# Performance work log

Measured on AMD Instinct MI355X. Metric: run time of the kernel, lower is better.

Reference implementation:

```python
import jax, jax.numpy as jnp
import numpy as np

B, C, H, W = 8, 64, 128, 128
K = 3            # deformable kernel size
DIL = 1          # dilation == padding for the deformable conv
OFF_K = 2 * (DIL + 1) + 1   # = 5, offset-conv kernel
OFF_PAD = DIL + 1            # = 2, same-padding for offset conv
KK = K * K


def setup_inputs() -> dict:
    key = jax.random.key(0)
    k1, k2, k3, k4 = jax.random.split(key, 4)
    x = jax.random.normal(k1, (B, C, H, W), dtype=jnp.float32)
    weights = jax.random.normal(k2, (C, C, K, K), dtype=jnp.float32) * 0.05
    offset_w = jax.random.normal(k3, (2 * KK, C, OFF_K, OFF_K), dtype=jnp.float32) * 0.02
    offset_b = jax.random.normal(k4, (2 * KK,), dtype=jnp.float32) * 0.01
    return {"x": x, "weights": weights, "offset_w": offset_w, "offset_b": offset_b}


def _deform_conv2d(x, weights, off):
    # x: [B,C,H,W]; weights: [O,C,K,K]; off: [B,2*KK,H,W] (dy,dx interleaved per tap)
    b, c, h, w = x.shape
    o = weights.shape[0]
    off = off.reshape(b, KK, 2, h, w)
    dy = off[:, :, 0]            # [B,KK,H,W]
    dx = off[:, :, 1]
    ti = jnp.arange(KK) // K     # kernel row per tap
    tj = jnp.arange(KK) % K      # kernel col per tap
    ygrid = jnp.arange(h, dtype=jnp.float32)
    xgrid = jnp.arange(w, dtype=jnp.float32)
    # sample position: out_pos - pad + tap*dilation + offset
    base_y = (ti * DIL - DIL).astype(jnp.float32)  # pad = DIL
    base_x = (tj * DIL - DIL).astype(jnp.float32)
    py = ygrid[None, None, :, None] + base_y[None, :, None, None] + dy  # [B,KK,H,W]
    px = xgrid[None, None, None, :] + base_x[None, :, None, None] + dx

    def sample_one(img, py_b, px_b):
        # img: [C,H,W]; py_b/px_b: [KK,H,W] -> [C,KK,H,W]
        y0 = jnp.floor(py_b)
        x0 = jnp.floor(px_b)
        fy = py_b - y0
        fx = px_b - x0
        y0i = y0.astype(jnp.int32)
        x0i = x0.astype(jnp.int32)

        def corner(yi, xi, wgt):
            valid = (yi >= 0) & (yi < h) & (xi >= 0) & (xi < w)
            v = img[:, jnp.clip(yi, 0, h - 1), jnp.clip(xi, 0, w - 1)]  # [C,KK,H,W]
            return v * (wgt * valid)[None]

        return (corner(y0i, x0i, (1 - fy) * (1 - fx))
                + corner(y0i, x0i + 1, (1 - fy) * fx)
                + corner(y0i + 1, x0i, fy * (1 - fx))
                + corner(y0i + 1, x0i + 1, fy * fx))

    sampled = jax.vmap(sample_one)(x, py, px)            # [B,C,KK,H,W]
    return jnp.einsum('bctyx,oct->boyx', sampled, weights.reshape(o, c, KK))


def reference(x, weights, offset_w, offset_b):
    # offset conv (same padding) + Hardtanh clamp to [-1,1]
    off = jax.lax.conv_general_dilated(
        x, offset_w, window_strides=(1, 1),
        padding=[(OFF_PAD, OFF_PAD), (OFF_PAD, OFF_PAD)],
        dimension_numbers=('NCHW', 'OIHW', 'NCHW'))
    off = off + offset_b[None, :, None, None]
    off = jnp.clip(off, -1.0, 1.0)
    return _deform_conv2d(x, weights, off)
```

## Files before the change

### kernel.cpp

```cpp
#include <hip/hip_runtime.h>

#define BB  8
#define CC  64
#define HH  128
#define WW  128
#define OCC 18
#define XP  133
#define SP  72
#define XTP 68

typedef __attribute__((ext_vector_type(8)))  short bf16x8;
typedef __attribute__((ext_vector_type(16))) float f32x16;

static __device__ __forceinline__ ushort f2bf(float f) {
    union { float f; unsigned u; } v; v.f = f;
    unsigned r = (v.u + 0x7FFFu + ((v.u >> 16) & 1u)) >> 16;
    return (ushort)r;
}
static __device__ __forceinline__ float bfu(unsigned u) {
    union { unsigned u; float f; } v; v.u = u; return v.f;
}

__global__ __launch_bounds__(256) void prep_kernel(
    const float* __restrict__ x, const float* __restrict__ w,
    const float* __restrict__ ow, ushort* __restrict__ XT,
    ushort* __restrict__ WAf, ushort* __restrict__ WDf)
{
    __shared__ ushort T[64 * XTP];
    const int tid = threadIdx.x;
    const int phys = blockIdx.x;

    if (phys >= 2 * BB * HH) {
        int id = phys - 2 * BB * HH;
        if (id < 200) {
            int idx = id * 256 + tid;
            int j  = idx & 7;
            int l  = (idx >> 3) & 63;
            int cs = (idx >> 9) & 3;
            int t  = idx >> 11;
            int oc = l & 31;
            int c  = cs * 16 + (l >> 5) * 8 + j;
            float v = (oc < OCC) ? ow[((size_t)(oc * CC + c)) * 25 + t] : 0.f;
            WAf[idx] = f2bf(v);
        } else {
            int idx = (id - 200) * 256 + tid;
            int j  = idx & 7;
            int l  = (idx >> 3) & 63;
            int cs = (idx >> 9) & 3;
            int mt = (idx >> 11) & 1;
            int t  = idx >> 12;
            int o  = mt * 32 + (l & 31);
            int c  = cs * 16 + (l >> 5) * 8 + j;
            WDf[idx] = f2bf(w[((size_t)(o * CC + c)) * 9 + t]);
        }
        return;
    }

    const int b    = phys & 7;
    const int idx  = phys >> 3;
    const int half = idx & 1;
    const int y    = idx >> 1;

    {
        int j = idx * 256 + tid;
        if (j < 5 * XP * 8) {
            int r   = j / (XP * 8);
            int off = j % (XP * 8);
            int yp  = (r < 2) ? r : (128 + r);
            ((uint4*)(XT + ((size_t)b * XP + yp) * XP * 64))[off] = make_uint4(0, 0, 0, 0);
        }
    }

    const int p   = tid & 63;
    const int ch4 = tid >> 6;
    const float* xb = x + (size_t)b * CC * HH * WW + (size_t)y * WW + half * 64;
#pragma unroll
    for (int i = 0; i < 16; i++) {
        int c = i * 4 + ch4;
        T[p * XTP + c] = f2bf(xb[(size_t)c * HH * WW + p]);
    }
    __syncthreads();

    ushort* orow = XT + (((size_t)b * XP + (y + 2)) * XP) * 64;

    if (half == 0) {
        if (tid < 16) {
            int col = tid >> 3;
            ((uint4*)(orow + (size_t)col * 64))[tid & 7] = make_uint4(0, 0, 0, 0);
        }
    } else {
        if (tid < 24) {
            int col = 130 + (tid >> 3);
            ((uint4*)(orow + (size_t)col * 64))[tid & 7] = make_uint4(0, 0, 0, 0);
        }
    }

#pragma unroll
    for (int g = 0; g < 2; g++) {
        int i2 = g * 256 + tid;
        int pl = i2 >> 3;
        int part = i2 & 7;
        uint2 lo = *(const uint2*)&T[pl * XTP + part * 8];
        uint2 hi = *(const uint2*)&T[pl * XTP + part * 8 + 4];
        uint4 wv; wv.x = lo.x; wv.y = lo.y; wv.z = hi.x; wv.w = hi.y;
        ((uint4*)(orow + ((size_t)(half * 64 + pl + 2)) * 64))[part] = wv;
    }
}

__global__ __launch_bounds__(256, 6) void fused_kernel(
    const ushort* __restrict__ XT, const ushort* __restrict__ WAf,
    const ushort* __restrict__ WDf, const float* __restrict__ ob,
    float* __restrict__ out)
{
    __shared__ __align__(16) char smem[68 * SP * 2];
    __shared__ float off_lds[OCC * 64];

    const int tid   = threadIdx.x;
    const int lane  = tid & 63;
    const int n     = lane & 31;
    const int h     = lane >> 5;
    const int w     = tid >> 6;
    const int ptile = w & 1;
    const int tset  = w >> 1;

    const int b    = blockIdx.x & 7;
    const int idx  = blockIdx.x >> 3;
    const int half = idx & 1;
    const int y    = idx >> 1;

    {
        ushort* XROW = (ushort*)smem;
        float*  red  = (float*)smem;
        f32x16 acc = {};
        const ushort* src0 = XT + (((size_t)b * XP + y) * XP + half * 64) * 64;

        for (int ky = 0; ky < 5; ky++) {
            if (ky) __syncthreads();
            const ushort* src = src0 + (size_t)ky * XP * 64;
            for (int i = tid; i < 68 * 8; i += 256) {
                int pl = i >> 3, ch = (i & 7) * 8;
                *(uint4*)&XROW[pl * SP + ch] = *(const uint4*)(src + (size_t)pl * 64 + ch);
            }
            __syncthreads();

#pragma unroll
            for (int kx = 0; kx < 5; kx++) {
                const int t = ky * 5 + kx;
                const ushort* bbase = &XROW[(ptile * 32 + n + kx) * SP + h * 8];
#pragma unroll
                for (int c2 = 0; c2 < 2; c2++) {
                    const int cs = tset * 2 + c2;
                    bf16x8 af = *(const bf16x8*)(WAf + (((size_t)t * 4 + cs) * 64 + lane) * 8);
                    bf16x8 bf = *(const bf16x8*)(bbase + cs * 16);
                    acc = __builtin_amdgcn_mfma_f32_32x32x16_bf16(af, bf, acc, 0, 0, 0);
                }
            }
        }
        __syncthreads();
        if (tset == 1) {
#pragma unroll
            for (int r = 0; r < 16; r++)
                red[ptile * 1024 + r * 64 + lane] = acc[r];
        }
        __syncthreads();
        if (tset == 0) {
#pragma unroll
            for (int r = 0; r < 16; r++) {
                int oc = (r & 3) + 8 * (r >> 2) + 4 * h;
                if (oc < OCC) {
                    float v = acc[r] + red[ptile * 1024 + r * 64 + lane] + ob[oc];
                    v = fminf(fmaxf(v, -1.f), 1.f);
                    off_lds[oc * 64 + ptile * 32 + n] = v;
                }
            }
        }
        __syncthreads();
    }

    ushort* S = (ushort*)smem;
    const int p   = tid >> 2;
    const int cs4 = (tid & 3) * 16;

    const int m0 = ptile * 32;
    const int n0 = tset * 32;

    f32x16 acc = {};
    const ushort* xtb = XT + (size_t)b * XP * XP * 64;

    for (int t = 0; t < 9; t++) {
        float dy = off_lds[(2 * t) * 64 + p];
        float dx = off_lds[(2 * t + 1) * 64 + p];
        float py = (float)(y + t / 3 - 1) + dy;
        float px = (float)(half * 64 + p + t % 3 - 1) + dx;
        float y0f = floorf(py), x0f = floorf(px);
        float fy = py - y0f, fx = px - x0f;
        int iy = (int)y0f + 2, ix = (int)x0f + 2;
        float w00 = (1.f - fy) * (1.f - fx), w01 = (1.f - fy) * fx;
        float w10 = fy * (1.f - fx),         w11 = fy * fx;

        const ushort* c00 = xtb + ((size_t)iy * XP + ix) * 64 + cs4;
        const ushort* c10 = c00 + XP * 64;

        uint4 q[8];
        q[0] = *(const uint4*)(c00);      q[1] = *(const uint4*)(c00 + 8);
        q[2] = *(const uint4*)(c00 + 64); q[3] = *(const uint4*)(c00 + 72);
        q[4] = *(const uint4*)(c10);      q[5] = *(const uint4*)(c10 + 8);
        q[6] = *(const uint4*)(c10 + 64); q[7] = *(const uint4*)(c10 + 72);

        __syncthreads();

#pragma unroll
        for (int m = 0; m < 2; m++) {
            unsigned o4[4];
#pragma unroll
            for (int j = 0; j < 4; j++) {
                unsigned u00 = ((const unsigned*)&q[m])[j];
                unsigned u01 = ((const unsigned*)&q[2 + m])[j];
                unsigned u10 = ((const unsigned*)&q[4 + m])[j];
                unsigned u11 = ((const unsigned*)&q[6 + m])[j];
                float lo = w00 * bfu(u00 << 16) + w01 * bfu(u01 << 16)
                         + w10 * bfu(u10 << 16) + w11 * bfu(u11 << 16);
                float hi = w00 * bfu(u00 & 0xffff0000u) + w01 * bfu(u01 & 0xffff0000u)
                         + w10 * bfu(u10 & 0xffff0000u) + w11 * bfu(u11 & 0xffff0000u);
                o4[j] = (unsigned)f2bf(lo) | ((unsigned)f2bf(hi) << 16);
            }
            *(uint4*)&S[p * SP + cs4 + m * 8] = *(uint4*)o4;
        }
        __syncthreads();

        const ushort* bp = &S[(n0 + n) * SP + h * 8];
#pragma unroll
        for (int cs = 0; cs < 4; cs++) {
            bf16x8 af = *(const bf16x8*)(WDf + ((((size_t)t * 2 + ptile) * 4 + cs) * 64 + lane) * 8);
            bf16x8 bf = *(const bf16x8*)(bp + cs * 16);
            acc = __builtin_amdgcn_mfma_f32_32x32x16_bf16(af, bf, acc, 0, 0, 0);
        }
    }

#pragma unroll
    for (int r = 0; r < 16; r++) {
        int o = m0 + (r & 3) + 8 * (r >> 2) + 4 * h;
        out[((size_t)(b * CC + o) * HH + y) * WW + half * 64 + n0 + n] = acc[r];
    }
}

extern "C" void kernel_launch(void* const* d_in, const int* in_sizes, int n_in,
                              void* d_out, int out_size, void* d_ws, size_t ws_size,
                              hipStream_t stream)
{
    const float* x  = (const float*)d_in[0];
    const float* w  = (const float*)d_in[1];
    const float* ow = (const float*)d_in[2];
    const float* ob = (const float*)d_in[3];
    float* out = (float*)d_out;

    ushort* XT  = (ushort*)d_ws;
    ushort* WAf = (ushort*)((char*)d_ws + 18113536);
    ushort* WDf = (ushort*)((char*)d_ws + 18215936);

    prep_kernel<<<2 * BB * HH + 344, 256, 0, stream>>>(x, w, ow, XT, WAf, WDf);
    fused_kernel<<<2 * BB * HH, 256, 0, stream>>>(XT, WAf, WDf, ob, out);
}
```

Measured before the change: 149.8 us.

## Double-buffer LDS and prefetch next tap/row loads in fused deformable conv

Splits shared memory into two buffers. In the offset-conv phase, the next input row is prefetched into registers while MFMAs run on the current row, and one barrier per row replaces two. The deformable-sampling loop also prefetches the next tap's four corner loads before the barrier, alternates LDS buffers, and packs the bilinear blend into 2-wide float math with a simpler round-half-up bf16 conversion. Costs are more registers and double the LDS (occupancy hint drops from 6 to 4 blocks). The rounding differs slightly from round-to-nearest-even.

```diff
diff --git a/kernel.cpp b/kernel.cpp
--- a/kernel.cpp
+++ b/kernel.cpp
@@ -11,6 +11,7 @@
 
 typedef __attribute__((ext_vector_type(8)))  short bf16x8;
 typedef __attribute__((ext_vector_type(16))) float f32x16;
+typedef __attribute__((ext_vector_type(2)))  float v2f;
 
 static __device__ __forceinline__ ushort f2bf(float f) {
     union { float f; unsigned u; } v; v.f = f;
@@ -19,6 +20,9 @@
 }
 static __device__ __forceinline__ float bfu(unsigned u) {
     union { unsigned u; float f; } v; v.u = u; return v.f;
+}
+static __device__ __forceinline__ unsigned uf(float f) {
+    union { float f; unsigned u; } v; v.f = f; return v.u;
 }
 
 __global__ __launch_bounds__(256) void prep_kernel(
@@ -107,12 +111,36 @@
     }
 }
 
-__global__ __launch_bounds__(256, 6) void fused_kernel(
+struct TapCtx { uint4 q[8]; float w00, w01, w10, w11; };
+
+static __device__ __forceinline__ void tap_load(
+    const ushort* __restrict__ xtb, const float* __restrict__ off_lds,
+    int y, int half, int p, int cs4, int t, TapCtx& c)
+{
+    float dy = off_lds[(2 * t) * 64 + p];
+    float dx = off_lds[(2 * t + 1) * 64 + p];
+    float py = (float)(y + t / 3 - 1) + dy;
+    float px = (float)(half * 64 + p + t % 3 - 1) + dx;
+    float y0f = floorf(py), x0f = floorf(px);
+    float fy = py - y0f, fx = px - x0f;
+    int iy = (int)y0f + 2, ix = (int)x0f + 2;
+    c.w00 = (1.f - fy) * (1.f - fx); c.w01 = (1.f - fy) * fx;
+    c.w10 = fy * (1.f - fx);         c.w11 = fy * fx;
+    const ushort* c00 = xtb + ((size_t)iy * XP + ix) * 64 + cs4;
+    const ushort* c10 = c00 + XP * 64;
+    c.q[0] = *(const uint4*)(c00);      c.q[1] = *(const uint4*)(c00 + 8);
+    c.q[2] = *(const uint4*)(c00 + 64); c.q[3] = *(const uint4*)(c00 + 72);
+    c.q[4] = *(const uint4*)(c10);      c.q[5] = *(const uint4*)(c10 + 8);
+    c.q[6] = *(const uint4*)(c10 + 64); c.q[7] = *(const uint4*)(c10 + 72);
+}
+
+__global__ __launch_bounds__(256, 4) void fused_kernel(
     const ushort* __restrict__ XT, const ushort* __restrict__ WAf,
     const ushort* __restrict__ WDf, const float* __restrict__ ob,
     float* __restrict__ out)
 {
-    __shared__ __align__(16) char smem[68 * SP * 2];
+    __shared__ __align__(16) char smem0[68 * SP * 2];
+    __shared__ __align__(16) char smem1[68 * SP * 2];
     __shared__ float off_lds[OCC * 64];
 
     const int tid   = threadIdx.x;
@@ -129,24 +157,39 @@
     const int y    = idx >> 1;
 
     {
-        ushort* XROW = (ushort*)smem;
-        float*  red  = (float*)smem;
+        ushort* XR[2] = { (ushort*)smem0, (ushort*)smem1 };
+        float*  red   = (float*)smem0;
         f32x16 acc = {};
-        const ushort* src0 = XT + (((size_t)b * XP + y) * XP + half * 64) * 64;
-
+        const uint4* srcb = (const uint4*)(XT + (((size_t)b * XP + y) * XP + half * 64) * 64);
+
+#pragma unroll
+        for (int k = 0; k < 3; k++) {
+            int i = tid + k * 256;
+            if (i < 544) {
+                uint4 v = srcb[i];
+                *(uint4*)&XR[0][(i >> 3) * SP + (i & 7) * 8] = v;
+            }
+        }
+        __syncthreads();
+
+#pragma unroll
         for (int ky = 0; ky < 5; ky++) {
-            if (ky) __syncthreads();
-            const ushort* src = src0 + (size_t)ky * XP * 64;
-            for (int i = tid; i < 68 * 8; i += 256) {
-                int pl = i >> 3, ch = (i & 7) * 8;
-                *(uint4*)&XROW[pl * SP + ch] = *(const uint4*)(src + (size_t)pl * 64 + ch);
-            }
-            __syncthreads();
+            ushort* Xc = XR[ky & 1];
+
+            uint4 pf[3];
+            if (ky < 4) {
+                const uint4* src = srcb + (size_t)(ky + 1) * XP * 8;
+#pragma unroll
+                for (int k = 0; k < 3; k++) {
+                    int i = tid + k * 256;
+                    if (i < 544) pf[k] = src[i];
+                }
+            }
 
 #pragma unroll
             for (int kx = 0; kx < 5; kx++) {
                 const int t = ky * 5 + kx;
-                const ushort* bbase = &XROW[(ptile * 32 + n + kx) * SP + h * 8];
+                const ushort* bbase = &Xc[(ptile * 32 + n + kx) * SP + h * 8];
 #pragma unroll
                 for (int c2 = 0; c2 < 2; c2++) {
                     const int cs = tset * 2 + c2;
@@ -155,8 +198,18 @@
                     acc = __builtin_amdgcn_mfma_f32_32x32x16_bf16(af, bf, acc, 0, 0, 0);
                 }
             }
-        }
-        __syncthreads();
+
+            if (ky < 4) {
+                ushort* Xn = XR[(ky + 1) & 1];
+#pragma unroll
+                for (int k = 0; k < 3; k++) {
+                    int i = tid + k * 256;
+                    if (i < 544) *(uint4*)&Xn[(i >> 3) * SP + (i & 7) * 8] = pf[k];
+                }
+            }
+            __syncthreads();
+        }
+
         if (tset == 1) {
 #pragma unroll
             for (int r = 0; r < 16; r++)
@@ -177,64 +230,55 @@
         __syncthreads();
     }
 
-    ushort* S = (ushort*)smem;
+    ushort* Sb[2] = { (ushort*)smem0, (ushort*)smem1 };
     const int p   = tid >> 2;
     const int cs4 = (tid & 3) * 16;
-
-    const int m0 = ptile * 32;
-    const int n0 = tset * 32;
+    const int m0  = ptile * 32;
+    const int n0  = tset * 32;
 
     f32x16 acc = {};
     const ushort* xtb = XT + (size_t)b * XP * XP * 64;
 
+    TapCtx cur, nxt;
+    tap_load(xtb, off_lds, y, half, p, cs4, 0, cur);
+
+#pragma unroll
     for (int t = 0; t < 9; t++) {
-        float dy = off_lds[(2 * t) * 64 + p];
-        float dx = off_lds[(2 * t + 1) * 64 + p];
-        float py = (float)(y + t / 3 - 1) + dy;
-        float px = (float)(half * 64 + p + t % 3 - 1) + dx;
-        float y0f = floorf(py), x0f = floorf(px);
-        float fy = py - y0f, fx = px - x0f;
-        int iy = (int)y0f + 2, ix = (int)x0f + 2;
-        float w00 = (1.f - fy) * (1.f - fx), w01 = (1.f - fy) * fx;
-        float w10 = fy * (1.f - fx),         w11 = fy * fx;
-
-        const ushort* c00 = xtb + ((size_t)iy * XP + ix) * 64 + cs4;
-        const ushort* c10 = c00 + XP * 64;
-
-        uint4 q[8];
-        q[0] = *(const uint4*)(c00);      q[1] = *(const uint4*)(c00 + 8);
-        q[2] = *(const uint4*)(c00 + 64); q[3] = *(const uint4*)(c00 + 72);
-        q[4] = *(const uint4*)(c10);      q[5] = *(const uint4*)(c10 + 8);
-        q[6] = *(const uint4*)(c10 + 64); q[7] = *(const uint4*)(c10 + 72);
-
-        __syncthreads();
+        ushort* St = Sb[t & 1];
 
 #pragma unroll
         for (int m = 0; m < 2; m++) {
             unsigned o4[4];
 #pragma unroll
             for (int j = 0; j < 4; j++) {
-                unsigned u00 = ((const unsigned*)&q[m])[j];
-                unsigned u01 = ((const unsigned*)&q[2 + m])[j];
-                unsigned u10 = ((const unsigned*)&q[4 + m])[j];
-                unsigned u11 = ((const unsigned*)&q[6 + m])[j];
-                float lo = w00 * bfu(u00 << 16) + w01 * bfu(u01 << 16)
-                         + w10 * bfu(u10 << 16) + w11 * bfu(u11 << 16);
-                float hi = w00 * bfu(u00 & 0xffff0000u) + w01 * bfu(u01 & 0xffff0000u)
-                         + w10 * bfu(u10 & 0xffff0000u) + w11 * bfu(u11 & 0xffff0000u);
-                o4[j] = (unsigned)f2bf(lo) | ((unsigned)f2bf(hi) << 16);
-            }
-            *(uint4*)&S[p * SP + cs4 + m * 8] = *(uint4*)o4;
-        }
+                unsigned u00 = ((const unsigned*)&cur.q[m])[j];
+                unsigned u01 = ((const unsigned*)&cur.q[2 + m])[j];
+                unsigned u10 = ((const unsigned*)&cur.q[4 + m])[j];
+                unsigned u11 = ((const unsigned*)&cur.q[6 + m])[j];
+                v2f a  = { bfu(u00 << 16), bfu(u00 & 0xffff0000u) };
+                v2f bb = { bfu(u01 << 16), bfu(u01 & 0xffff0000u) };
+                v2f cc = { bfu(u10 << 16), bfu(u10 & 0xffff0000u) };
+                v2f dd = { bfu(u11 << 16), bfu(u11 & 0xffff0000u) };
+                v2f r = a * cur.w00 + bb * cur.w01 + cc * cur.w10 + dd * cur.w11;
+                unsigned rl = uf(r.x) + 0x8000u;
+                unsigned rh = uf(r.y) + 0x8000u;
+                o4[j] = (rl >> 16) | (rh & 0xffff0000u);
+            }
+            *(uint4*)&St[p * SP + cs4 + m * 8] = *(uint4*)o4;
+        }
+
+        if (t < 8) tap_load(xtb, off_lds, y, half, p, cs4, t + 1, nxt);
+
         __syncthreads();
 
-        const ushort* bp = &S[(n0 + n) * SP + h * 8];
+        const ushort* bp = &St[(n0 + n) * SP + h * 8];
 #pragma unroll
         for (int cs = 0; cs < 4; cs++) {
             bf16x8 af = *(const bf16x8*)(WDf + ((((size_t)t * 2 + ptile) * 4 + cs) * 64 + lane) * 8);
             bf16x8 bf = *(const bf16x8*)(bp + cs * 16);
             acc = __builtin_amdgcn_mfma_f32_32x32x16_bf16(af, bf, acc, 0, 0, 0);
         }
+        cur = nxt;
     }
 
 #pragma unroll
```

After: 160.1 us. 1.07x slower.
